# Kernel optimization log

Measured on AMD Instinct MI355X. Metric: run time of the kernel, lower is better.

## Reference

```python
import jax, jax.numpy as jnp
import numpy as np

H = 16  # hidden size (fixed by the module)


def setup_inputs() -> dict:
    key = jax.random.key(0)
    ks = jax.random.split(key, 12)
    B, T = 512, 4096
    x = jax.random.normal(ks[0], (B, T, 1), dtype=jnp.float32)
    h0 = jax.random.normal(ks[1], (B, H), dtype=jnp.float32)
    c0 = jax.random.normal(ks[2], (B, H), dtype=jnp.float32)
    s = 1.0 / np.sqrt(H)
    # PyTorch LSTM params, gate order (i, f, g, o)
    W_ih = jax.random.uniform(ks[3], (4 * H, 1), jnp.float32, -s, s)
    W_hh = jax.random.uniform(ks[4], (4 * H, H), jnp.float32, -s, s)
    b_ih = jax.random.uniform(ks[5], (4 * H,), jnp.float32, -s, s)
    b_hh = jax.random.uniform(ks[6], (4 * H,), jnp.float32, -s, s)
    # MLP head: Linear(16,16) then Linear(16,1)
    W1 = jax.random.uniform(ks[7], (H, H), jnp.float32, -s, s)
    b1 = jax.random.uniform(ks[8], (H,), jnp.float32, -s, s)
    W2 = jax.random.uniform(ks[9], (1, H), jnp.float32, -s, s)
    b2 = jax.random.uniform(ks[10], (1,), jnp.float32, -s, s)
    return {"x": x, "h0": h0, "c0": c0, "W_ih": W_ih, "W_hh": W_hh,
            "b_ih": b_ih, "b_hh": b_hh, "W1": W1, "b1": b1,
            "W2": W2, "b2": b2, "batch_size": B}


def _lstm(x, h0, c0, W_ih, W_hh, b):
    # x: [B,T,1] -> scan over time; gate order i,f,g,o (PyTorch)
    xs = jnp.swapaxes(x, 0, 1)  # [T,B,1]
    # precompute input projection for all timesteps: [T,B,4H]
    xg = jnp.einsum('tbi,gi->tbg', xs, W_ih) + b

    def step(carry, xg_t):
        h, c = carry
        gates = xg_t + h @ W_hh.T  # [B,4H]
        i, f, g, o = jnp.split(gates, 4, axis=-1)
        c = jax.nn.sigmoid(f) * c + jax.nn.sigmoid(i) * jnp.tanh(g)
        h = jax.nn.sigmoid(o) * jnp.tanh(c)
        return (h, c), h

    _, hs = jax.lax.scan(step, (h0, c0), xg)
    return jnp.swapaxes(hs, 0, 1)  # [B,T,H]


def reference(x, h0, c0, W_ih, W_hh, b_ih, b_hh, W1, b1, W2, b2, batch_size):
    hs = _lstm(x, h0, c0, W_ih, W_hh, b_ih + b_hh)  # [B,T,H]
    y = jax.nn.relu(hs)
    y = jax.nn.relu(y @ W1.T + b1)
    y = jnp.tanh(y @ W2.T + b2)  # [B,T,1]
    T = x.shape[1]
    out = y.reshape(batch_size, 1, T)
    return jnp.cumsum(out, axis=1)  # cumsum over singleton dim (faithful to source)
```

## Files before the change

### kernel.cpp

```cpp
#include <hip/hip_runtime.h>
#include <cstdint>
#include <cstddef>

#define LOG2E 1.4426950408889634f

__device__ __forceinline__ float fexp2(float x) {
#if __has_builtin(__builtin_amdgcn_exp2f)
  return __builtin_amdgcn_exp2f(x);
#else
  return exp2f(x);
#endif
}

__device__ __forceinline__ float frcp(float x) {
#if __has_builtin(__builtin_amdgcn_rcpf)
  return __builtin_amdgcn_rcpf(x);
#else
  return 1.0f / x;
#endif
}

__device__ __forceinline__ float rl(float v, int l) {
  return __int_as_float(__builtin_amdgcn_readlane(__float_as_int(v), l));
}

template <int CTRL>
__device__ __forceinline__ float dppmov(float x) {
  return __int_as_float(
      __builtin_amdgcn_update_dpp(0, __float_as_int(x), CTRL, 0xf, 0xf, true));
}
#define DPP_QUAD_XOR1 0xB1
#define DPP_QUAD_XOR2 0x4E
#define DPP_HALF_MIRR 0x141
#define DPP_MIRR 0x140
#define DPP_ROR1 0x121
#define DPP_ROR4 0x124
#define DPP_ROR8 0x128
#define DPP_ROR12 0x12C

__device__ __forceinline__ float sum16(float x) {
#if __has_builtin(__builtin_amdgcn_permlane16_swap)
  auto r = __builtin_amdgcn_permlane16_swap(__float_as_uint(x),
                                            __float_as_uint(x), false, false);
  return __uint_as_float(r[0]) + __uint_as_float(r[1]);
#else
  float a = x, b = x;
  asm("v_permlane16_swap_b32 %0, %1" : "+v"(a), "+v"(b));
  return a + b;
#endif
}
__device__ __forceinline__ float sum32(float x) {
#if __has_builtin(__builtin_amdgcn_permlane32_swap)
  auto r = __builtin_amdgcn_permlane32_swap(__float_as_uint(x),
                                            __float_as_uint(x), false, false);
  return __uint_as_float(r[0]) + __uint_as_float(r[1]);
#else
  float a = x, b = x;
  asm("v_permlane32_swap_b32 %0, %1" : "+v"(a), "+v"(b));
  return a + b;
#endif
}
__device__ __forceinline__ float mul32(float x) {
#if __has_builtin(__builtin_amdgcn_permlane32_swap)
  auto r = __builtin_amdgcn_permlane32_swap(__float_as_uint(x),
                                            __float_as_uint(x), false, false);
  return __uint_as_float(r[0]) * __uint_as_float(r[1]);
#else
  float a = x, b = x;
  asm("v_permlane32_swap_b32 %0, %1" : "+v"(a), "+v"(b));
  return a * b;
#endif
}

__global__ __launch_bounds__(64) void lstm_gen_kernel(
    const float* __restrict__ x, const float* __restrict__ h0,
    const float* __restrict__ c0, const float* __restrict__ W_ih,
    const float* __restrict__ W_hh, const float* __restrict__ b_ih,
    const float* __restrict__ b_hh, const float* __restrict__ W1,
    const float* __restrict__ b1, const float* __restrict__ W2,
    const float* __restrict__ b2, float* __restrict__ out, int T) {
  const int b = blockIdx.x;
  const int lane = threadIdx.x;
  const int j = lane & 15;
  const int type = lane >> 4;
  const bool rowodd = (lane & 16) != 0;
  const bool isF = (type == 1);
  const bool isO = (type == 3);

  const float sk = (type == 2) ? (-2.0f * LOG2E) : (-LOG2E);
  const float Aact = (type == 2) ? 2.0f : 1.0f;
  const float Bact = (type == 2) ? -1.0f : 0.0f;

  float w[16];
#pragma unroll
  for (int jj = 0; jj < 16; ++jj) w[jj] = W_hh[lane * 16 + jj] * sk;
  const float wi = W_ih[lane] * sk;
  const float bk = (b_ih[lane] + b_hh[lane]) * sk;

  float w1rot[16];
#pragma unroll
  for (int r = 0; r < 16; ++r) w1rot[r] = W1[j * 16 + ((j - r) & 15)];
  const float b1r = b1[j];
  const float w2r = W2[j];
  const float b2v = b2[0];

  float h = h0[b * 16 + j];
  float c = c0[b * 16 + j];

  const float* xrow = x + (size_t)b * (size_t)T;
  float* orow = out + (size_t)b * (size_t)T;
  const int T4 = T >> 2;
  const float4* xrow4 = (const float4*)xrow;

  float4 xa = xrow4[0];
  float4 xb = xrow4[(1 < T4) ? 1 : 0];
  float4 xc2 = xrow4[(2 < T4) ? 2 : 0];

#pragma unroll 1
  for (int t4i = 0; t4i < T4; ++t4i) {
    const float4 xcur = xa;
    xa = xb;
    xb = xc2;
    int nidx = t4i + 3;
    nidx = (nidx < T4) ? nidx : (T4 - 1);
    xc2 = xrow4[nidx];

    float hq = 0.0f;

#pragma unroll
    for (int tt = 0; tt < 4; ++tt) {
      const float xv = (tt == 0) ? xcur.x : (tt == 1) ? xcur.y
                        : (tt == 2) ? xcur.z : xcur.w;
      float a0 = fmaf(wi, xv, bk);
      float a1 = 0.0f, a2 = 0.0f, a3 = 0.0f;
#pragma unroll
      for (int jj = 0; jj < 16; jj += 4) {
        a0 = fmaf(rl(h, jj + 0), w[jj + 0], a0);
        a1 = fmaf(rl(h, jj + 1), w[jj + 1], a1);
        a2 = fmaf(rl(h, jj + 2), w[jj + 2], a2);
        a3 = fmaf(rl(h, jj + 3), w[jj + 3], a3);
      }
      const float gacc = (a0 + a1) + (a2 + a3);
      const float act = fmaf(Aact, frcp(1.0f + fexp2(gacc)), Bact);

      const float m = mul32(act);
      const float IG_all = sum16(rowodd ? 0.0f : m);
      const float F_all = sum32(sum16(isF ? act : 0.0f));
      const float O_all = sum32(sum16(isO ? act : 0.0f));

      c = fmaf(F_all, c, IG_all);
      const float tc = fmaf(-2.0f, frcp(1.0f + fexp2(c * (2.0f * LOG2E))), 1.0f);
      h = O_all * tc;
      hq = (type == tt) ? h : hq;
    }

    const float cur = fmaxf(hq, 0.0f);
    float r0v = cur;
    float r4v = dppmov<DPP_ROR4>(cur);
    float r8v = dppmov<DPP_ROR8>(cur);
    float r12v = dppmov<DPP_ROR12>(cur);
    float m0 = fmaf(r0v, w1rot[0], b1r);
    float m1 = r4v * w1rot[4];
    float m2 = r8v * w1rot[8];
    float m3 = r12v * w1rot[12];
#pragma unroll
    for (int r = 1; r < 4; ++r) {
      r0v = dppmov<DPP_ROR1>(r0v);
      r4v = dppmov<DPP_ROR1>(r4v);
      r8v = dppmov<DPP_ROR1>(r8v);
      r12v = dppmov<DPP_ROR1>(r12v);
      m0 = fmaf(r0v, w1rot[r], m0);
      m1 = fmaf(r4v, w1rot[4 + r], m1);
      m2 = fmaf(r8v, w1rot[8 + r], m2);
      m3 = fmaf(r12v, w1rot[12 + r], m3);
    }
    const float y2 = (m0 + m1) + (m2 + m3);

    float v = fmaxf(y2, 0.0f) * w2r;
    v += dppmov<DPP_QUAD_XOR1>(v);
    v += dppmov<DPP_QUAD_XOR2>(v);
    v += dppmov<DPP_HALF_MIRR>(v);
    v += dppmov<DPP_MIRR>(v);
    const float z = v + b2v;
    const float y3 = fmaf(-2.0f, frcp(1.0f + fexp2(z * (2.0f * LOG2E))), 1.0f);

    if (j == 0) orow[t4i * 4 + type] = y3;
  }
}

extern "C" void kernel_launch(void* const* d_in, const int* in_sizes, int n_in,
                              void* d_out, int out_size, void* d_ws,
                              size_t ws_size, hipStream_t stream) {
  (void)n_in; (void)d_ws; (void)ws_size;
  const float* x = (const float*)d_in[0];
  const float* h0 = (const float*)d_in[1];
  const float* c0 = (const float*)d_in[2];
  const float* W_ih = (const float*)d_in[3];
  const float* W_hh = (const float*)d_in[4];
  const float* b_ih = (const float*)d_in[5];
  const float* b_hh = (const float*)d_in[6];
  const float* W1 = (const float*)d_in[7];
  const float* b1 = (const float*)d_in[8];
  const float* W2 = (const float*)d_in[9];
  const float* b2 = (const float*)d_in[10];

  const int B = in_sizes[1] / 16;
  const int T = in_sizes[0] / (B > 0 ? B : 1);

  lstm_gen_kernel<<<B, 64, 0, stream>>>(x, h0, c0, W_ih, W_hh, b_ih, b_hh,
                                        W1, b1, W2, b2, (float*)d_out, T);
}
```

Measured before the change: 1.167 ms.

## Interleave four independent batch rows per wavefront for ILP

```diff
diff --git a/kernel.cpp b/kernel.cpp
--- a/kernel.cpp
+++ b/kernel.cpp
@@ -3,6 +3,7 @@
 #include <cstddef>
 
 #define LOG2E 1.4426950408889634f
+#define NC 4
 
 __device__ __forceinline__ float fexp2(float x) {
 #if __has_builtin(__builtin_amdgcn_exp2f)
@@ -78,8 +79,7 @@
     const float* __restrict__ W_hh, const float* __restrict__ b_ih,
     const float* __restrict__ b_hh, const float* __restrict__ W1,
     const float* __restrict__ b1, const float* __restrict__ W2,
-    const float* __restrict__ b2, float* __restrict__ out, int T) {
-  const int b = blockIdx.x;
+    const float* __restrict__ b2, float* __restrict__ out, int T, int B) {
   const int lane = threadIdx.x;
   const int j = lane & 15;
   const int type = lane >> 4;
@@ -104,87 +104,114 @@
   const float w2r = W2[j];
   const float b2v = b2[0];
 
-  float h = h0[b * 16 + j];
-  float c = c0[b * 16 + j];
-
-  const float* xrow = x + (size_t)b * (size_t)T;
-  float* orow = out + (size_t)b * (size_t)T;
+  const int b0 = blockIdx.x * NC;
   const int T4 = T >> 2;
-  const float4* xrow4 = (const float4*)xrow;
-
-  float4 xa = xrow4[0];
-  float4 xb = xrow4[(1 < T4) ? 1 : 0];
-  float4 xc2 = xrow4[(2 < T4) ? 2 : 0];
+
+  float h[NC], c[NC];
+  const float4* xrow4[NC];
+  float* orow[NC];
+  bool live[NC];
+#pragma unroll
+  for (int cc = 0; cc < NC; ++cc) {
+    int bc = b0 + cc;
+    live[cc] = (bc < B);
+    bc = live[cc] ? bc : (B - 1);
+    h[cc] = h0[bc * 16 + j];
+    c[cc] = c0[bc * 16 + j];
+    xrow4[cc] = (const float4*)(x + (size_t)bc * (size_t)T);
+    orow[cc] = out + (size_t)bc * (size_t)T;
+  }
+
+  float4 xa[NC], xb[NC], xc2[NC];
+#pragma unroll
+  for (int cc = 0; cc < NC; ++cc) {
+    xa[cc] = xrow4[cc][0];
+    xb[cc] = xrow4[cc][(1 < T4) ? 1 : 0];
+    xc2[cc] = xrow4[cc][(2 < T4) ? 2 : 0];
+  }
 
 #pragma unroll 1
   for (int t4i = 0; t4i < T4; ++t4i) {
-    const float4 xcur = xa;
-    xa = xb;
-    xb = xc2;
     int nidx = t4i + 3;
     nidx = (nidx < T4) ? nidx : (T4 - 1);
-    xc2 = xrow4[nidx];
-
-    float hq = 0.0f;
+    float4 xcur[NC];
+#pragma unroll
+    for (int cc = 0; cc < NC; ++cc) {
+      xcur[cc] = xa[cc];
+      xa[cc] = xb[cc];
+      xb[cc] = xc2[cc];
+      xc2[cc] = xrow4[cc][nidx];
+    }
+
+    float hq[NC];
+#pragma unroll
+    for (int cc = 0; cc < NC; ++cc) hq[cc] = 0.0f;
 
 #pragma unroll
     for (int tt = 0; tt < 4; ++tt) {
-      const float xv = (tt == 0) ? xcur.x : (tt == 1) ? xcur.y
-                        : (tt == 2) ? xcur.z : xcur.w;
-      float a0 = fmaf(wi, xv, bk);
-      float a1 = 0.0f, a2 = 0.0f, a3 = 0.0f;
-#pragma unroll
-      for (int jj = 0; jj < 16; jj += 4) {
-        a0 = fmaf(rl(h, jj + 0), w[jj + 0], a0);
-        a1 = fmaf(rl(h, jj + 1), w[jj + 1], a1);
-        a2 = fmaf(rl(h, jj + 2), w[jj + 2], a2);
-        a3 = fmaf(rl(h, jj + 3), w[jj + 3], a3);
+#pragma unroll
+      for (int cc = 0; cc < NC; ++cc) {
+        const float xv = (tt == 0) ? xcur[cc].x : (tt == 1) ? xcur[cc].y
+                          : (tt == 2) ? xcur[cc].z : xcur[cc].w;
+        float a0 = fmaf(wi, xv, bk);
+        float a1 = 0.0f, a2 = 0.0f, a3 = 0.0f;
+#pragma unroll
+        for (int jj = 0; jj < 16; jj += 4) {
+          a0 = fmaf(rl(h[cc], jj + 0), w[jj + 0], a0);
+          a1 = fmaf(rl(h[cc], jj + 1), w[jj + 1], a1);
+          a2 = fmaf(rl(h[cc], jj + 2), w[jj + 2], a2);
+          a3 = fmaf(rl(h[cc], jj + 3), w[jj + 3], a3);
+        }
+        const float gacc = (a0 + a1) + (a2 + a3);
+        const float act = fmaf(Aact, frcp(1.0f + fexp2(gacc)), Bact);
+
+        const float m = mul32(act);
+        const float IG_all = sum16(rowodd ? 0.0f : m);
+        const float F_all = sum32(sum16(isF ? act : 0.0f));
+        const float O_all = sum32(sum16(isO ? act : 0.0f));
+
+        c[cc] = fmaf(F_all, c[cc], IG_all);
+        const float tc =
+            fmaf(-2.0f, frcp(1.0f + fexp2(c[cc] * (2.0f * LOG2E))), 1.0f);
+        h[cc] = O_all * tc;
+        hq[cc] = (type == tt) ? h[cc] : hq[cc];
       }
-      const float gacc = (a0 + a1) + (a2 + a3);
-      const float act = fmaf(Aact, frcp(1.0f + fexp2(gacc)), Bact);
-
-      const float m = mul32(act);
-      const float IG_all = sum16(rowodd ? 0.0f : m);
-      const float F_all = sum32(sum16(isF ? act : 0.0f));
-      const float O_all = sum32(sum16(isO ? act : 0.0f));
-
-      c = fmaf(F_all, c, IG_all);
-      const float tc = fmaf(-2.0f, frcp(1.0f + fexp2(c * (2.0f * LOG2E))), 1.0f);
-      h = O_all * tc;
-      hq = (type == tt) ? h : hq;
     }
 
-    const float cur = fmaxf(hq, 0.0f);
-    float r0v = cur;
-    float r4v = dppmov<DPP_ROR4>(cur);
-    float r8v = dppmov<DPP_ROR8>(cur);
-    float r12v = dppmov<DPP_ROR12>(cur);
-    float m0 = fmaf(r0v, w1rot[0], b1r);
-    float m1 = r4v * w1rot[4];
-    float m2 = r8v * w1rot[8];
-    float m3 = r12v * w1rot[12];
-#pragma unroll
-    for (int r = 1; r < 4; ++r) {
-      r0v = dppmov<DPP_ROR1>(r0v);
-      r4v = dppmov<DPP_ROR1>(r4v);
-      r8v = dppmov<DPP_ROR1>(r8v);
-      r12v = dppmov<DPP_ROR1>(r12v);
-      m0 = fmaf(r0v, w1rot[r], m0);
-      m1 = fmaf(r4v, w1rot[4 + r], m1);
-      m2 = fmaf(r8v, w1rot[8 + r], m2);
-      m3 = fmaf(r12v, w1rot[12 + r], m3);
+#pragma unroll
+    for (int cc = 0; cc < NC; ++cc) {
+      const float cur = fmaxf(hq[cc], 0.0f);
+      float r0v = cur;
+      float r4v = dppmov<DPP_ROR4>(cur);
+      float r8v = dppmov<DPP_ROR8>(cur);
+      float r12v = dppmov<DPP_ROR12>(cur);
+      float m0 = fmaf(r0v, w1rot[0], b1r);
+      float m1 = r4v * w1rot[4];
+      float m2 = r8v * w1rot[8];
+      float m3 = r12v * w1rot[12];
+#pragma unroll
+      for (int r = 1; r < 4; ++r) {
+        r0v = dppmov<DPP_ROR1>(r0v);
+        r4v = dppmov<DPP_ROR1>(r4v);
+        r8v = dppmov<DPP_ROR1>(r8v);
+        r12v = dppmov<DPP_ROR1>(r12v);
+        m0 = fmaf(r0v, w1rot[r], m0);
+        m1 = fmaf(r4v, w1rot[4 + r], m1);
+        m2 = fmaf(r8v, w1rot[8 + r], m2);
+        m3 = fmaf(r12v, w1rot[12 + r], m3);
+      }
+      const float y2 = (m0 + m1) + (m2 + m3);
+
+      float v = fmaxf(y2, 0.0f) * w2r;
+      v += dppmov<DPP_QUAD_XOR1>(v);
+      v += dppmov<DPP_QUAD_XOR2>(v);
+      v += dppmov<DPP_HALF_MIRR>(v);
+      v += dppmov<DPP_MIRR>(v);
+      const float z = v + b2v;
+      const float y3 = fmaf(-2.0f, frcp(1.0f + fexp2(z * (2.0f * LOG2E))), 1.0f);
+
+      if (j == 0 && live[cc]) orow[cc][t4i * 4 + type] = y3;
     }
-    const float y2 = (m0 + m1) + (m2 + m3);
-
-    float v = fmaxf(y2, 0.0f) * w2r;
-    v += dppmov<DPP_QUAD_XOR1>(v);
-    v += dppmov<DPP_QUAD_XOR2>(v);
-    v += dppmov<DPP_HALF_MIRR>(v);
-    v += dppmov<DPP_MIRR>(v);
-    const float z = v + b2v;
-    const float y3 = fmaf(-2.0f, frcp(1.0f + fexp2(z * (2.0f * LOG2E))), 1.0f);
-
-    if (j == 0) orow[t4i * 4 + type] = y3;
   }
 }
 
@@ -206,7 +233,8 @@
 
   const int B = in_sizes[1] / 16;
   const int T = in_sizes[0] / (B > 0 ? B : 1);
-
-  lstm_gen_kernel<<<B, 64, 0, stream>>>(x, h0, c0, W_ih, W_hh, b_ih, b_hh,
-                                        W1, b1, W2, b2, (float*)d_out, T);
-}
+  const int grid = (B + NC - 1) / NC;
+
+  lstm_gen_kernel<<<grid, 64, 0, stream>>>(x, h0, c0, W_ih, W_hh, b_ih, b_hh,
+                                           W1, b1, W2, b2, (float*)d_out, T, B);
+}
```

Result: slower. 3.430 ms (+194.0%).
